# Kernel tuning notes

Measured on AMD Instinct MI355X. Metric: run time of the kernel, lower is better.

## Reference

```python
import jax, jax.numpy as jnp
import numpy as np

B, S, D, H = 4, 2048, 768, 12
HD = D // H

def rope_cos_sin(seq_len, head_dim, dtype=jnp.float32):
    inv_freq = 1.0 / (10000.0 ** (jnp.arange(0, head_dim, 2, dtype=jnp.float32) / head_dim))
    ang = jnp.arange(seq_len, dtype=jnp.float32)[:, None] * inv_freq[None, :]  # (S, HD/2)
    cos = jnp.concatenate([jnp.cos(ang), jnp.cos(ang)], axis=-1).astype(dtype)  # (S, HD)
    sin = jnp.concatenate([jnp.sin(ang), jnp.sin(ang)], axis=-1).astype(dtype)
    return cos, sin

def rotate_half(x):
    x1, x2 = jnp.split(x, 2, axis=-1)
    return jnp.concatenate([-x2, x1], axis=-1)

def setup_inputs() -> dict:
    key = jax.random.key(0)
    k0, k1, k2, k3, k4 = jax.random.split(key, 5)
    s = 0.02
    return {
        "embeds": jax.random.normal(k0, (B, S, D), jnp.float32),
        "Wq": jax.random.normal(k1, (D, D), jnp.float32) * s,
        "Wk": jax.random.normal(k2, (D, D), jnp.float32) * s,
        "Wv": jax.random.normal(k3, (D, D), jnp.float32) * s,
        "Wo": jax.random.normal(k4, (D, D), jnp.float32) * s,
        "bo": jnp.zeros((D,), jnp.float32),
    }

def reference(embeds, Wq, Wk, Wv, Wo, bo):
    b, n, d = embeds.shape
    scale = 1.0 / np.sqrt(HD)
    # projections (torch Linear: x @ W.T), reshape to (b, H, n, HD)
    def proj(W):
        return (embeds @ W.T).reshape(b, n, H, HD).transpose(0, 2, 1, 3)
    q, k, v = proj(Wq), proj(Wk), proj(Wv)
    cos, sin = rope_cos_sin(n, HD)  # (n, HD)
    cos, sin = cos[None, None], sin[None, None]
    q = q * cos + rotate_half(q) * sin
    k = k * cos + rotate_half(k) * sin
    scores = jnp.einsum('bhqd,bhkd->bhqk', q, k)
    causal = jnp.triu(jnp.ones((n, n), bool), k=1)
    scores = jnp.where(causal, -jnp.inf, scores) * scale
    attn = jax.nn.softmax(scores, axis=-1)
    ctx = jnp.einsum('bhqk,bhkd->bhqd', attn, v)
    ctx = ctx.transpose(0, 2, 1, 3).reshape(b, n, d)
    return ctx @ Wo.T + bo
```

## Files before the change

kernel.cpp:

```cpp
#include <hip/hip_runtime.h>
#include <hip/hip_bf16.h>

using bf16x8 = __attribute__((ext_vector_type(8))) short;
using f32x4  = __attribute__((ext_vector_type(4))) float;

#define DEVI __device__ __forceinline__

static constexpr int S_LEN = 2048, D_MODEL = 768, NH = 12, HDIM = 64;
static constexpr float QSCALE = 0.125f * 1.4426950408889634f;

DEVI unsigned short f2bf(float x) {
    unsigned u = __builtin_bit_cast(unsigned, x);
    u += 0x7fffu + ((u >> 16) & 1u);
    return (unsigned short)(u >> 16);
}

DEVI unsigned short bf16c(float x) {
    return __builtin_bit_cast(unsigned short, __float2bfloat16(x));
}

#define GLL16(gsrc, ldst) __builtin_amdgcn_global_load_lds( \
    (const __attribute__((address_space(1))) void*)(gsrc),  \
    (__attribute__((address_space(3))) void*)(ldst), 16, 0, 0)

DEVI bf16x8 lds_frag(const unsigned short* lds, int row, int cb) {
    return *(const bf16x8*)((const char*)lds + row * 128 + (cb ^ ((row & 7) << 4)));
}

__global__ __launch_bounds__(256) void prep_kernel(
        const float* __restrict__ emb, const float* __restrict__ Wq, const float* __restrict__ Wk,
        const float* __restrict__ Wv, const float* __restrict__ Wo,
        unsigned short* __restrict__ emb_bf, unsigned short* __restrict__ wq_bf,
        unsigned short* __restrict__ wk_bf, unsigned short* __restrict__ wv_bf,
        unsigned short* __restrict__ wo_bf, float* __restrict__ cos_t, float* __restrict__ sin_t) {
    constexpr int NE4 = 1572864;
    constexpr int NW4 = 147456;
    constexpr int EMB_BLOCKS = NE4 / 256;
    constexpr int W_BLOCKS   = 4 * NW4 / 256;
    int bx = blockIdx.x;
    if (bx < EMB_BLOCKS) {
        int i = bx * 256 + threadIdx.x;
        float4 v = reinterpret_cast<const float4*>(emb)[i];
        ushort4 o; o.x = f2bf(v.x); o.y = f2bf(v.y); o.z = f2bf(v.z); o.w = f2bf(v.w);
        reinterpret_cast<ushort4*>(emb_bf)[i] = o;
    } else if (bx < EMB_BLOCKS + W_BLOCKS) {
        int i = (bx - EMB_BLOCKS) * 256 + threadIdx.x;
        int m = i / NW4, off = i - m * NW4;
        const float* s = (m == 0) ? Wq : (m == 1) ? Wk : (m == 2) ? Wv : Wo;
        unsigned short* d = (m == 0) ? wq_bf : (m == 1) ? wk_bf : (m == 2) ? wv_bf : wo_bf;
        float4 v = reinterpret_cast<const float4*>(s)[off];
        ushort4 o; o.x = f2bf(v.x); o.y = f2bf(v.y); o.z = f2bf(v.z); o.w = f2bf(v.w);
        reinterpret_cast<ushort4*>(d)[off] = o;
    } else {
        int idx = (bx - EMB_BLOCKS - W_BLOCKS) * 256 + threadIdx.x;
        int hd = idx >> 11, spos = idx & 2047;
        float inv = exp2f(-(float)hd * (13.287712379549449f / 32.0f));
        float ang = (float)spos * inv;
        cos_t[idx] = cosf(ang);
        sin_t[idx] = sinf(ang);
    }
}

DEVI void stage128x64(const unsigned short* __restrict__ g, unsigned short* lds,
                      int ldg, int row0, int k0, int wave, int lane) {
    int rl = lane >> 3;
    int cb = (lane & 7) << 4;
    #pragma unroll
    for (int i = 0; i < 4; ++i) {
        int r = wave * 32 + i * 8 + rl;
        const char* src = (const char*)(g + (size_t)(row0 + r) * ldg + k0) + (cb ^ ((r & 7) << 4));
        GLL16(src, lds + (wave * 32 + i * 8) * 64);
    }
}

DEVI void gemm_core(const unsigned short* __restrict__ Ag, const unsigned short* __restrict__ Bg,
                    int m0, int n0, int K, int lda, int ldb,
                    unsigned short* As, unsigned short* Bs, f32x4 acc[4][4]) {
    int tid = threadIdx.x, wave = tid >> 6, lane = tid & 63;
    int wr = wave >> 1, wc = wave & 1, lrow = lane & 15, lk = lane >> 4;
    #pragma unroll
    for (int mi = 0; mi < 4; ++mi)
        #pragma unroll
        for (int ni = 0; ni < 4; ++ni) acc[mi][ni] = f32x4{0.f, 0.f, 0.f, 0.f};
    for (int k0 = 0; k0 < K; k0 += 64) {
        stage128x64(Ag, As, lda, m0, k0, wave, lane);
        stage128x64(Bg, Bs, ldb, n0, k0, wave, lane);
        __syncthreads();
        #pragma unroll
        for (int kk = 0; kk < 2; ++kk) {
            bf16x8 a[4], b[4];
            #pragma unroll
            for (int mi = 0; mi < 4; ++mi) a[mi] = lds_frag(As, wr * 64 + mi * 16 + lrow, kk * 64 + lk * 16);
            #pragma unroll
            for (int ni = 0; ni < 4; ++ni) b[ni] = lds_frag(Bs, wc * 64 + ni * 16 + lrow, kk * 64 + lk * 16);
            __builtin_amdgcn_s_setprio(1);
            #pragma unroll
            for (int mi = 0; mi < 4; ++mi)
                #pragma unroll
                for (int ni = 0; ni < 4; ++ni)
                    acc[mi][ni] = __builtin_amdgcn_mfma_f32_16x16x32_bf16(a[mi], b[ni], acc[mi][ni], 0, 0, 0);
            __builtin_amdgcn_s_setprio(0);
        }
        __syncthreads();
    }
}

__global__ __launch_bounds__(256) void qkv_kernel(
        const unsigned short* __restrict__ Xg,
        const unsigned short* __restrict__ Wqg, const unsigned short* __restrict__ Wkg,
        const unsigned short* __restrict__ Wvg,
        const float* __restrict__ cos_t, const float* __restrict__ sin_t,
        unsigned short* __restrict__ Qo, unsigned short* __restrict__ Ko,
        unsigned short* __restrict__ Vt) {
    __shared__ unsigned short sbuf[128 * 128];
    unsigned short* As = sbuf;
    unsigned short* Bs = sbuf + 128 * 64;
    int z = blockIdx.z;
    const unsigned short* Wg = (z == 0) ? Wqg : ((z == 1) ? Wkg : Wvg);
    int m0 = blockIdx.x * 128, n0 = blockIdx.y * 128;
    f32x4 acc[4][4];
    gemm_core(Xg, Wg, m0, n0, D_MODEL, D_MODEL, D_MODEL, As, Bs, acc);

    int tid = threadIdx.x, wave = tid >> 6, lane = tid & 63;
    int wr = wave >> 1, wc = wave & 1, lrow = lane & 15, lk = lane >> 4;

    if (z < 2) {
        unsigned short* O = (z == 0) ? Qo : Ko;
        float qs = (z == 0) ? QSCALE : 1.0f;
        int h = blockIdx.y * 2 + wc;
        #pragma unroll
        for (int mi = 0; mi < 4; ++mi) {
            int m_base = m0 + wr * 64 + mi * 16 + lk * 4;
            int bb = m_base >> 11, sp0 = m_base & 2047;
            size_t obase = ((size_t)(bb * NH + h) * S_LEN + sp0) * HDIM;
            #pragma unroll
            for (int nf = 0; nf < 2; ++nf) {
                int hd = nf * 16 + lrow;
                float4 c4 = *(const float4*)(cos_t + hd * 2048 + sp0);
                float4 s4 = *(const float4*)(sin_t + hd * 2048 + sp0);
                #pragma unroll
                for (int r = 0; r < 4; ++r) {
                    float c = ((const float*)&c4)[r], sn = ((const float*)&s4)[r];
                    float x1 = acc[mi][nf][r], x2 = acc[mi][nf + 2][r];
                    O[obase + (size_t)r * HDIM + hd]      = f2bf((x1 * c - x2 * sn) * qs);
                    O[obase + (size_t)r * HDIM + hd + 32] = f2bf((x2 * c + x1 * sn) * qs);
                }
            }
        }
    } else {
        unsigned short* T = sbuf;
        #pragma unroll
        for (int mi = 0; mi < 4; ++mi)
            #pragma unroll
            for (int nt = 0; nt < 4; ++nt) {
                int hd  = wc * 64 + nt * 16 + lrow;
                int sp0 = wr * 64 + mi * 16 + lk * 4;
                ushort4 pk;
                pk.x = f2bf(acc[mi][nt][0]); pk.y = f2bf(acc[mi][nt][1]);
                pk.z = f2bf(acc[mi][nt][2]); pk.w = f2bf(acc[mi][nt][3]);
                *(ushort4*)((char*)T + ((hd * 256 + sp0 * 2) ^ ((hd & 7) << 4))) = pk;
            }
        __syncthreads();
        int hd = tid >> 1, half = tid & 1;
        int h  = blockIdx.y * 2 + (hd >> 6), hdh = hd & 63;
        int bb = m0 >> 11, sp_abs = (m0 & 2047) + half * 64;
        unsigned short* dst = Vt + ((size_t)(bb * NH + h) * HDIM + hdh) * S_LEN + sp_abs;
        #pragma unroll
        for (int j = 0; j < 8; ++j) {
            bf16x8 v = *(const bf16x8*)((const char*)T +
                        ((hd * 256 + half * 128 + j * 16) ^ ((hd & 7) << 4)));
            *(bf16x8*)((char*)dst + j * 16) = v;
        }
    }
}

DEVI void attn_stage(const unsigned short* __restrict__ Kb, const unsigned short* __restrict__ Vt,
                     unsigned short* Ksb, unsigned short* Vsb,
                     int bh, int kv0, int wave, int lane) {
    int rl = lane >> 3, cb = (lane & 7) << 4;
    #pragma unroll
    for (int i = 0; i < 2; ++i) {
        int r = wave * 16 + i * 8 + rl;
        int scb = cb ^ ((r & 7) << 4);
        const char* srck = (const char*)(Kb + ((size_t)bh * S_LEN + kv0 + r) * HDIM) + scb;
        GLL16(srck, Ksb + (wave * 16 + i * 8) * 64);
        const char* srcv = (const char*)(Vt + ((size_t)bh * HDIM + r) * S_LEN + kv0) + scb;
        GLL16(srcv, Vsb + (wave * 16 + i * 8) * 64);
    }
}

DEVI void do_qkt_sw(const bf16x8 (&kf)[2][4], bf16x8 qf0, bf16x8 qf1, f32x4 (&sc)[4]) {
    #pragma unroll
    for (int nt = 0; nt < 4; ++nt) sc[nt] = f32x4{0.f, 0.f, 0.f, 0.f};
    __builtin_amdgcn_s_setprio(1);
    #pragma unroll
    for (int kk = 0; kk < 2; ++kk) {
        bf16x8 qf = kk ? qf1 : qf0;
        #pragma unroll
        for (int nt = 0; nt < 4; ++nt)
            sc[nt] = __builtin_amdgcn_mfma_f32_16x16x32_bf16(kf[kk][nt], qf, sc[nt], 0, 0, 0);
    }
    __builtin_amdgcn_s_setprio(0);
}

template <bool DIAG>
DEVI void do_softmax_sw(const f32x4 (&sc)[4], unsigned short* Pw, f32x4 o[4],
                        float& mrow, float& lsum, int lrow, int lk, int qrel) {
    float t[16];
    #pragma unroll
    for (int nt = 0; nt < 4; ++nt)
        #pragma unroll
        for (int r = 0; r < 4; ++r) {
            float v = sc[nt][r];
            if (DIAG && (nt * 16 + lk * 4 + r > qrel)) v = -__builtin_inff();
            t[nt * 4 + r] = v;
        }
    float mx = fmaxf(fmaxf(t[0], t[1]), t[2]);
    mx = fmaxf(fmaxf(mx, t[3]), t[4]);
    mx = fmaxf(fmaxf(mx, t[5]), t[6]);
    mx = fmaxf(fmaxf(mx, t[7]), t[8]);
    mx = fmaxf(fmaxf(mx, t[9]), t[10]);
    mx = fmaxf(fmaxf(mx, t[11]), t[12]);
    mx = fmaxf(fmaxf(mx, t[13]), t[14]);
    mx = fmaxf(mx, t[15]);
    mx = fmaxf(mx, __shfl_xor(mx, 16, 64));
    mx = fmaxf(mx, __shfl_xor(mx, 32, 64));
    if (!__all(mx <= mrow + 8.0f)) {
        float mnew = fmaxf(mrow, mx);
        float alpha = exp2f(mrow - mnew);
        mrow = mnew;
        lsum *= alpha;
        #pragma unroll
        for (int nt = 0; nt < 4; ++nt) o[nt] *= alpha;
    }
    float ps = 0.f;
    #pragma unroll
    for (int nt = 0; nt < 4; ++nt) {
        float p0 = exp2f(t[nt * 4 + 0] - mrow), p1 = exp2f(t[nt * 4 + 1] - mrow);
        float p2 = exp2f(t[nt * 4 + 2] - mrow), p3 = exp2f(t[nt * 4 + 3] - mrow);
        ps += (p0 + p1) + (p2 + p3);
        ushort4 pk;
        pk.x = bf16c(p0); pk.y = bf16c(p1); pk.z = bf16c(p2); pk.w = bf16c(p3);
        *(ushort4*)((char*)Pw + lrow * 128 + (((nt * 16 + lk * 4) * 2) ^ ((lrow & 7) << 4))) = pk;
    }
    ps += __shfl_xor(ps, 16, 64);
    ps += __shfl_xor(ps, 32, 64);
    lsum += ps;
}

DEVI void do_pv_sw(const unsigned short* Vs, const unsigned short* Pw, f32x4 o[4],
                   int lrow, int lk) {
    __builtin_amdgcn_s_setprio(1);
    #pragma unroll
    for (int kk = 0; kk < 2; ++kk) {
        bf16x8 pf = lds_frag(Pw, lrow, kk * 64 + lk * 16);
        #pragma unroll
        for (int nt = 0; nt < 4; ++nt) {
            bf16x8 vf = lds_frag(Vs, nt * 16 + lrow, kk * 64 + lk * 16);
            o[nt] = __builtin_amdgcn_mfma_f32_16x16x32_bf16(vf, pf, o[nt], 0, 0, 0);
        }
    }
    __builtin_amdgcn_s_setprio(0);
}

DEVI void attn_epilogue(const f32x4 o[4], float lsum, int qt, int bh,
                        unsigned short* __restrict__ Ctx, int lrow, int lk, int wave) {
    float inv = 1.0f / lsum;
    int b = bh / NH, h = bh % NH;
    int spos = qt * 64 + wave * 16 + lrow;
    size_t base = ((size_t)(b * S_LEN + spos)) * D_MODEL + h * HDIM;
    #pragma unroll
    for (int nt = 0; nt < 4; ++nt) {
        ushort4 pk;
        pk.x = bf16c(o[nt][0] * inv); pk.y = bf16c(o[nt][1] * inv);
        pk.z = bf16c(o[nt][2] * inv); pk.w = bf16c(o[nt][3] * inv);
        *(ushort4*)(Ctx + base + nt * 16 + lk * 4) = pk;
    }
}

__global__ __launch_bounds__(256, 3) void attn_kernel(
        const unsigned short* __restrict__ Q, const unsigned short* __restrict__ Kb,
        const unsigned short* __restrict__ Vt, unsigned short* __restrict__ Ctx) {
    __shared__ unsigned short Ks[2][64 * 64], Vs[2][64 * 64], Ps[4][16 * 64];
    int id = blockIdx.x;
    int n  = (id & 7) * 96 + (id >> 3);
    int bh = n >> 4;
    int pj = n & 15;
    int qa = pj, qb = 31 - pj;
    int tid = threadIdx.x, wave = tid >> 6, lane = tid & 63;
    int lrow = lane & 15, lk = lane >> 4;
    int qrel = wave * 16 + lrow;

    const unsigned short* qpa = Q + ((size_t)bh * S_LEN + qa * 64 + qrel) * HDIM;
    const unsigned short* qpb = Q + ((size_t)bh * S_LEN + qb * 64 + qrel) * HDIM;
    bf16x8 qfa0 = *(const bf16x8*)(qpa + lk * 8);
    bf16x8 qfa1 = *(const bf16x8*)(qpa + 32 + lk * 8);
    bf16x8 qfb0 = *(const bf16x8*)(qpb + lk * 8);
    bf16x8 qfb1 = *(const bf16x8*)(qpb + 32 + lk * 8);

    f32x4 oa[4], ob[4];
    float ma = -__builtin_inff(), la = 0.f, mb = -__builtin_inff(), lb = 0.f;
    #pragma unroll
    for (int nt = 0; nt < 4; ++nt) { oa[nt] = f32x4{0.f, 0.f, 0.f, 0.f}; ob[nt] = f32x4{0.f, 0.f, 0.f, 0.f}; }

    attn_stage(Kb, Vt, Ks[0], Vs[0], bh, 0, wave, lane);
    int cur = 0;
    f32x4 sc[4];
    for (int kt = 0; kt <= qb; ++kt) {
        __syncthreads();
        if (kt < qb) attn_stage(Kb, Vt, Ks[cur ^ 1], Vs[cur ^ 1], bh, (kt + 1) * 64, wave, lane);

        bf16x8 kf[2][4];
        #pragma unroll
        for (int kk = 0; kk < 2; ++kk)
            #pragma unroll
            for (int nt = 0; nt < 4; ++nt)
                kf[kk][nt] = lds_frag(Ks[cur], nt * 16 + lrow, kk * 64 + lk * 16);

        if (kt <= qa) {
            do_qkt_sw(kf, qfa0, qfa1, sc);
            if (kt == qa) do_softmax_sw<true >(sc, Ps[wave], oa, ma, la, lrow, lk, qrel);
            else          do_softmax_sw<false>(sc, Ps[wave], oa, ma, la, lrow, lk, qrel);
            do_pv_sw(Vs[cur], Ps[wave], oa, lrow, lk);
        }
        do_qkt_sw(kf, qfb0, qfb1, sc);
        if (kt == qb) do_softmax_sw<true >(sc, Ps[wave], ob, mb, lb, lrow, lk, qrel);
        else          do_softmax_sw<false>(sc, Ps[wave], ob, mb, lb, lrow, lk, qrel);
        do_pv_sw(Vs[cur], Ps[wave], ob, lrow, lk);
        cur ^= 1;
    }

    attn_epilogue(oa, la, qa, bh, Ctx, lrow, lk, wave);
    attn_epilogue(ob, lb, qb, bh, Ctx, lrow, lk, wave);
}

__global__ __launch_bounds__(256) void outproj_kernel(
        const unsigned short* __restrict__ Cg, const unsigned short* __restrict__ Wog,
        const float* __restrict__ bo, float* __restrict__ Out) {
    __shared__ unsigned short As[128 * 64], Bs[128 * 64];
    int m0 = blockIdx.x * 128, n0 = blockIdx.y * 128;
    f32x4 acc[4][4];
    gemm_core(Cg, Wog, m0, n0, D_MODEL, D_MODEL, D_MODEL, As, Bs, acc);

    int tid = threadIdx.x, wave = tid >> 6, lane = tid & 63;
    int wr = wave >> 1, wc = wave & 1, lrow = lane & 15, lk = lane >> 4;
    #pragma unroll
    for (int mi = 0; mi < 4; ++mi)
        #pragma unroll
        for (int r = 0; r < 4; ++r) {
            int m = m0 + wr * 64 + mi * 16 + lk * 4 + r;
            #pragma unroll
            for (int nt = 0; nt < 4; ++nt) {
                int n = n0 + wc * 64 + nt * 16 + lrow;
                Out[(size_t)m * D_MODEL + n] = acc[mi][nt][r] + bo[n];
            }
        }
}

extern "C" void kernel_launch(void* const* d_in, const int* in_sizes, int n_in,
                              void* d_out, int out_size, void* d_ws, size_t ws_size,
                              hipStream_t stream) {
    const float* embeds = (const float*)d_in[0];
    const float* Wq = (const float*)d_in[1];
    const float* Wk = (const float*)d_in[2];
    const float* Wv = (const float*)d_in[3];
    const float* Wo = (const float*)d_in[4];
    const float* bo = (const float*)d_in[5];
    float* out = (float*)d_out;

    const size_t NE = (size_t)4 * 2048 * 768;
    const size_t NW = (size_t)768 * 768;

    unsigned short* ws     = (unsigned short*)d_ws;
    unsigned short* emb_bf = ws;
    unsigned short* wq_bf  = emb_bf + NE;
    unsigned short* wk_bf  = wq_bf + NW;
    unsigned short* wv_bf  = wk_bf + NW;
    unsigned short* wo_bf  = wv_bf + NW;
    unsigned short* qb     = wo_bf + NW;
    unsigned short* kb     = qb + NE;
    unsigned short* vt     = kb + NE;
    float* cos_t = (float*)(vt + NE);
    float* sin_t = cos_t + 2048 * 32;
    unsigned short* ctx = emb_bf;

    prep_kernel<<<dim3(8704), 256, 0, stream>>>(embeds, Wq, Wk, Wv, Wo,
                                                emb_bf, wq_bf, wk_bf, wv_bf, wo_bf,
                                                cos_t, sin_t);
    qkv_kernel<<<dim3(64, 6, 3), 256, 0, stream>>>(emb_bf, wq_bf, wk_bf, wv_bf,
                                                   cos_t, sin_t, qb, kb, vt);
    attn_kernel<<<dim3(768), 256, 0, stream>>>(qb, kb, vt, ctx);
    outproj_kernel<<<dim3(64, 6), 256, 0, stream>>>(ctx, wo_bf, bo, out);
}
```

Baseline: 150.3 us.

## Split attention into one Q tile per block and swizzle QKV grid mapping

```diff
diff --git a/kernel.cpp b/kernel.cpp
--- a/kernel.cpp
+++ b/kernel.cpp
@@ -115,9 +115,12 @@
     __shared__ unsigned short sbuf[128 * 128];
     unsigned short* As = sbuf;
     unsigned short* Bs = sbuf + 128 * 64;
-    int z = blockIdx.z;
+    int bid = blockIdx.x;
+    int swz = (bid & 7) * 144 + (bid >> 3);
+    int x = swz / 18, rem = swz - x * 18;
+    int y = rem % 6, z = rem / 6;
     const unsigned short* Wg = (z == 0) ? Wqg : ((z == 1) ? Wkg : Wvg);
-    int m0 = blockIdx.x * 128, n0 = blockIdx.y * 128;
+    int m0 = x * 128, n0 = y * 128;
     f32x4 acc[4][4];
     gemm_core(Xg, Wg, m0, n0, D_MODEL, D_MODEL, D_MODEL, As, Bs, acc);
 
@@ -127,7 +130,7 @@
     if (z < 2) {
         unsigned short* O = (z == 0) ? Qo : Ko;
         float qs = (z == 0) ? QSCALE : 1.0f;
-        int h = blockIdx.y * 2 + wc;
+        int h = y * 2 + wc;
         #pragma unroll
         for (int mi = 0; mi < 4; ++mi) {
             int m_base = m0 + wr * 64 + mi * 16 + lk * 4;
@@ -162,7 +165,7 @@
             }
         __syncthreads();
         int hd = tid >> 1, half = tid & 1;
-        int h  = blockIdx.y * 2 + (hd >> 6), hdh = hd & 63;
+        int h  = y * 2 + (hd >> 6), hdh = hd & 63;
         int bb = m0 >> 11, sp_abs = (m0 & 2047) + half * 64;
         unsigned short* dst = Vt + ((size_t)(bb * NH + h) * HDIM + hdh) * S_LEN + sp_abs;
         #pragma unroll
@@ -189,7 +192,8 @@
     }
 }
 
-DEVI void do_qkt_sw(const bf16x8 (&kf)[2][4], bf16x8 qf0, bf16x8 qf1, f32x4 (&sc)[4]) {
+DEVI void do_qkt_lds(const unsigned short* Ks, bf16x8 qf0, bf16x8 qf1, f32x4 (&sc)[4],
+                     int lrow, int lk) {
     #pragma unroll
     for (int nt = 0; nt < 4; ++nt) sc[nt] = f32x4{0.f, 0.f, 0.f, 0.f};
     __builtin_amdgcn_s_setprio(1);
@@ -197,8 +201,10 @@
     for (int kk = 0; kk < 2; ++kk) {
         bf16x8 qf = kk ? qf1 : qf0;
         #pragma unroll
-        for (int nt = 0; nt < 4; ++nt)
-            sc[nt] = __builtin_amdgcn_mfma_f32_16x16x32_bf16(kf[kk][nt], qf, sc[nt], 0, 0, 0);
+        for (int nt = 0; nt < 4; ++nt) {
+            bf16x8 kf = lds_frag(Ks, nt * 16 + lrow, kk * 64 + lk * 16);
+            sc[nt] = __builtin_amdgcn_mfma_f32_16x16x32_bf16(kf, qf, sc[nt], 0, 0, 0);
+        }
     }
     __builtin_amdgcn_s_setprio(0);
 }
@@ -278,60 +284,44 @@
     }
 }
 
-__global__ __launch_bounds__(256, 3) void attn_kernel(
+__global__ __launch_bounds__(256, 4) void attn_kernel(
         const unsigned short* __restrict__ Q, const unsigned short* __restrict__ Kb,
         const unsigned short* __restrict__ Vt, unsigned short* __restrict__ Ctx) {
     __shared__ unsigned short Ks[2][64 * 64], Vs[2][64 * 64], Ps[4][16 * 64];
     int id = blockIdx.x;
-    int n  = (id & 7) * 96 + (id >> 3);
-    int bh = n >> 4;
-    int pj = n & 15;
-    int qa = pj, qb = 31 - pj;
+    int n  = (id & 7) * 192 + (id >> 3);
+    int bh = n >> 5;
+    int qt = 31 - (n & 31);
     int tid = threadIdx.x, wave = tid >> 6, lane = tid & 63;
     int lrow = lane & 15, lk = lane >> 4;
     int qrel = wave * 16 + lrow;
 
-    const unsigned short* qpa = Q + ((size_t)bh * S_LEN + qa * 64 + qrel) * HDIM;
-    const unsigned short* qpb = Q + ((size_t)bh * S_LEN + qb * 64 + qrel) * HDIM;
-    bf16x8 qfa0 = *(const bf16x8*)(qpa + lk * 8);
-    bf16x8 qfa1 = *(const bf16x8*)(qpa + 32 + lk * 8);
-    bf16x8 qfb0 = *(const bf16x8*)(qpb + lk * 8);
-    bf16x8 qfb1 = *(const bf16x8*)(qpb + 32 + lk * 8);
-
-    f32x4 oa[4], ob[4];
-    float ma = -__builtin_inff(), la = 0.f, mb = -__builtin_inff(), lb = 0.f;
-    #pragma unroll
-    for (int nt = 0; nt < 4; ++nt) { oa[nt] = f32x4{0.f, 0.f, 0.f, 0.f}; ob[nt] = f32x4{0.f, 0.f, 0.f, 0.f}; }
+    const unsigned short* qp = Q + ((size_t)bh * S_LEN + qt * 64 + qrel) * HDIM;
+    bf16x8 qf0 = *(const bf16x8*)(qp + lk * 8);
+    bf16x8 qf1 = *(const bf16x8*)(qp + 32 + lk * 8);
+
+    f32x4 o[4];
+    float m = -__builtin_inff(), l = 0.f;
+    #pragma unroll
+    for (int nt = 0; nt < 4; ++nt) o[nt] = f32x4{0.f, 0.f, 0.f, 0.f};
 
     attn_stage(Kb, Vt, Ks[0], Vs[0], bh, 0, wave, lane);
     int cur = 0;
     f32x4 sc[4];
-    for (int kt = 0; kt <= qb; ++kt) {
+    for (int kt = 0; kt < qt; ++kt) {
         __syncthreads();
-        if (kt < qb) attn_stage(Kb, Vt, Ks[cur ^ 1], Vs[cur ^ 1], bh, (kt + 1) * 64, wave, lane);
-
-        bf16x8 kf[2][4];
-        #pragma unroll
-        for (int kk = 0; kk < 2; ++kk)
-            #pragma unroll
-            for (int nt = 0; nt < 4; ++nt)
-                kf[kk][nt] = lds_frag(Ks[cur], nt * 16 + lrow, kk * 64 + lk * 16);
-
-        if (kt <= qa) {
-            do_qkt_sw(kf, qfa0, qfa1, sc);
-            if (kt == qa) do_softmax_sw<true >(sc, Ps[wave], oa, ma, la, lrow, lk, qrel);
-            else          do_softmax_sw<false>(sc, Ps[wave], oa, ma, la, lrow, lk, qrel);
-            do_pv_sw(Vs[cur], Ps[wave], oa, lrow, lk);
-        }
-        do_qkt_sw(kf, qfb0, qfb1, sc);
-        if (kt == qb) do_softmax_sw<true >(sc, Ps[wave], ob, mb, lb, lrow, lk, qrel);
-        else          do_softmax_sw<false>(sc, Ps[wave], ob, mb, lb, lrow, lk, qrel);
-        do_pv_sw(Vs[cur], Ps[wave], ob, lrow, lk);
+        attn_stage(Kb, Vt, Ks[cur ^ 1], Vs[cur ^ 1], bh, (kt + 1) * 64, wave, lane);
+        do_qkt_lds(Ks[cur], qf0, qf1, sc, lrow, lk);
+        do_softmax_sw<false>(sc, Ps[wave], o, m, l, lrow, lk, qrel);
+        do_pv_sw(Vs[cur], Ps[wave], o, lrow, lk);
         cur ^= 1;
     }
-
-    attn_epilogue(oa, la, qa, bh, Ctx, lrow, lk, wave);
-    attn_epilogue(ob, lb, qb, bh, Ctx, lrow, lk, wave);
+    __syncthreads();
+    do_qkt_lds(Ks[cur], qf0, qf1, sc, lrow, lk);
+    do_softmax_sw<true>(sc, Ps[wave], o, m, l, lrow, lk, qrel);
+    do_pv_sw(Vs[cur], Ps[wave], o, lrow, lk);
+
+    attn_epilogue(o, l, qt, bh, Ctx, lrow, lk, wave);
 }
 
 __global__ __launch_bounds__(256) void outproj_kernel(
@@ -387,8 +377,8 @@
     prep_kernel<<<dim3(8704), 256, 0, stream>>>(embeds, Wq, Wk, Wv, Wo,
                                                 emb_bf, wq_bf, wk_bf, wv_bf, wo_bf,
                                                 cos_t, sin_t);
-    qkv_kernel<<<dim3(64, 6, 3), 256, 0, stream>>>(emb_bf, wq_bf, wk_bf, wv_bf,
-                                                   cos_t, sin_t, qb, kb, vt);
-    attn_kernel<<<dim3(768), 256, 0, stream>>>(qb, kb, vt, ctx);
+    qkv_kernel<<<dim3(1152), 256, 0, stream>>>(emb_bf, wq_bf, wk_bf, wv_bf,
+                                               cos_t, sin_t, qb, kb, vt);
+    attn_kernel<<<dim3(1536), 256, 0, stream>>>(qb, kb, vt, ctx);
     outproj_kernel<<<dim3(64, 6), 256, 0, stream>>>(ctx, wo_bf, bo, out);
 }
```

After: 153.8 us. 1.02x slower.
